# Optimization experiments

Measured on AMD Instinct MI355X. Metric: run time of the kernel, lower is better.

The kernel has to match this reference:

```python
import jax, jax.numpy as jnp
import numpy as np

N = 100000
E = 400000
G = 2000  # number of graphs in batch
IN_DIM = 32
H = 192
L = 4
EPS = 1e-5


def setup_inputs() -> dict:
    key = jax.random.key(0)
    ks = jax.random.split(key, 20)
    x = jax.random.normal(ks[0], (N, IN_DIM), jnp.float32)
    edge_src = jax.random.randint(ks[1], (E,), 0, N, jnp.int32)
    edge_dst = jax.random.randint(ks[2], (E,), 0, N, jnp.int32)
    batch = jnp.sort(jax.random.randint(ks[3], (N,), 0, G, jnp.int32))
    s_in = 1.0 / np.sqrt(IN_DIM)
    s_h = 1.0 / np.sqrt(H)
    return {
        "x": x,
        "edge_src": edge_src,
        "edge_dst": edge_dst,
        "batch": batch,
        # layer 0 (in_dim -> H); weights stored [in, out]
        "Wrel0": jax.random.uniform(ks[4], (IN_DIM, H), jnp.float32, -s_in, s_in),
        "brel0": jax.random.uniform(ks[5], (H,), jnp.float32, -s_in, s_in),
        "Wroot0": jax.random.uniform(ks[6], (IN_DIM, H), jnp.float32, -s_in, s_in),
        # layers 1..3 stacked (H -> H)
        "Wrel": jax.random.uniform(ks[7], (L - 1, H, H), jnp.float32, -s_h, s_h),
        "brel": jax.random.uniform(ks[8], (L - 1, H), jnp.float32, -s_h, s_h),
        "Wroot": jax.random.uniform(ks[9], (L - 1, H, H), jnp.float32, -s_h, s_h),
        # batchnorm affine params for all 4 layers
        "gamma": jnp.ones((L, H), jnp.float32),
        "beta": jnp.zeros((L, H), jnp.float32),
        # head MLP and output
        "Wh1": jax.random.uniform(ks[10], (H, H), jnp.float32, -s_h, s_h),
        "bh1": jax.random.uniform(ks[11], (H,), jnp.float32, -s_h, s_h),
        "Wh2": jax.random.uniform(ks[12], (H, H), jnp.float32, -s_h, s_h),
        "bh2": jax.random.uniform(ks[13], (H,), jnp.float32, -s_h, s_h),
        "Wout": jax.random.uniform(ks[14], (H, 1), jnp.float32, -s_h, s_h),
        "bout": jax.random.uniform(ks[15], (1,), jnp.float32, -s_h, s_h),
    }


def _rel_conv(x, edge_src, edge_dst, Wrel, brel, Wroot):
    # message: lin_rel(x_j); applying the linear at node level first is the
    # same math as per-edge (linear commutes with gather) and cheaper.
    h = x @ Wrel + brel                      # [N, out]
    agg = jax.ops.segment_sum(h[edge_src], edge_dst, num_segments=N)
    return agg + x @ Wroot


def _bn_relu(h, g, b):
    # BatchNorm1d in training mode: batch stats over node dim, biased var
    mu = h.mean(axis=0)
    var = jnp.var(h, axis=0)
    h = (h - mu) * jax.lax.rsqrt(var + EPS) * g + b
    return jax.nn.relu(h)


def reference(x, edge_src, edge_dst, batch, Wrel0, brel0, Wroot0,
              Wrel, brel, Wroot, gamma, beta, Wh1, bh1, Wh2, bh2, Wout, bout):
    h = _bn_relu(_rel_conv(x, edge_src, edge_dst, Wrel0, brel0, Wroot0),
                 gamma[0], beta[0])
    for i in range(L - 1):
        h = _bn_relu(_rel_conv(h, edge_src, edge_dst, Wrel[i], brel[i], Wroot[i]),
                     gamma[i + 1], beta[i + 1])
    # global mean pool over graphs
    sums = jax.ops.segment_sum(h, batch, num_segments=G)          # [G, H]
    cnt = jax.ops.segment_sum(jnp.ones((N,), h.dtype), batch, num_segments=G)
    g = sums / jnp.maximum(cnt, 1.0)[:, None]
    # head MLP (dropout is identity at eval) + output linear
    g = jax.nn.relu(g @ Wh1 + bh1) @ Wh2 + bh2
    return g @ Wout + bout                                        # [G, 1]
```

## Files before the change

kernel.cpp:

```cpp
#include <hip/hip_runtime.h>

#define HDIM 192
#define EPS 1e-5f

typedef __attribute__((ext_vector_type(8))) _Float16 half8;
typedef __attribute__((ext_vector_type(4))) float floatx4;

__device__ __forceinline__ float h2f(ushort u) {
    union { ushort u; _Float16 h; } c; c.u = u; return (float)c.h;
}
__device__ __forceinline__ ushort f2h(float x) {
    _Float16 h = (_Float16)x;
    union { _Float16 h; ushort u; } c; c.h = h; return c.u;
}
__device__ __forceinline__ uint4 pack8(const ushort* h) {
    uint4 p;
    p.x = h[0] | ((uint)h[1] << 16); p.y = h[2] | ((uint)h[3] << 16);
    p.z = h[4] | ((uint)h[5] << 16); p.w = h[6] | ((uint)h[7] << 16);
    return p;
}

__device__ __forceinline__ void gload_lds16(const ushort* g, ushort* l) {
    __builtin_amdgcn_global_load_lds(
        (const __attribute__((address_space(1))) unsigned int*)g,
        (__attribute__((address_space(3))) unsigned int*)l, 16, 0, 0);
}

#define WAITV0() asm volatile("s_waitcnt vmcnt(0)" ::: "memory")


struct PrepArgs {
    const float* src[6];
    ushort*      dst[6];
    int K[6];
    int off[7];
};

__global__ __launch_bounds__(256) void prep_all_k(PrepArgs a)
{
    int idx = blockIdx.x * 256 + threadIdx.x;
    if (idx >= a.off[6]) return;
    int i = 0;
    #pragma unroll
    for (int t = 1; t < 6; ++t) if (idx >= a.off[t]) i = t;
    int r = idx - a.off[i];
    int K = a.K[i];
    int perMat = (K >> 5) * 12 * 64;
    int mat = r / perMat;
    r -= mat * perMat;
    int lane = r & 63;
    int ct = (r >> 6) % 12;
    int kc = r / (12 * 64);
    int col = ct * 16 + (lane & 15);
    int kb  = kc * 32 + (lane >> 4) * 8;
    const float* Wm = a.src[i] + (size_t)mat * K * HDIM;
    ushort* base = a.dst[i] + (size_t)mat * K * HDIM;
    size_t o = (size_t)kc * 6144 + (size_t)(ct * 64 + lane) * 8;
    #pragma unroll
    for (int j = 0; j < 8; ++j)
        base[o + j] = f2h(Wm[(size_t)(kb + j) * HDIM + col]);
}

__global__ __launch_bounds__(256) void conv_half_k(
    const float* __restrict__ src, ushort* __restrict__ dst, int R, int C)
{
    int OC = C >> 3;
    int idx = blockIdx.x * 256 + threadIdx.x;
    if (idx >= R * OC) return;
    int r = idx / OC;
    int o = idx - r * OC;
    float4 v0 = ((const float4*)(src + (size_t)r * C + o * 8))[0];
    float4 v1 = ((const float4*)(src + (size_t)r * C + o * 8))[1];
    float v[8] = {v0.x, v0.y, v0.z, v0.w, v1.x, v1.y, v1.z, v1.w};
    ushort h[8];
    #pragma unroll
    for (int t = 0; t < 8; ++t) h[t] = f2h(v[t]);
    *(uint4*)(dst + (size_t)r * C + o * 8) = pack8(h);
}

template<bool DUAL, bool RELU, bool DEG, bool STATS, bool BNIN, int NKC>
__global__ __launch_bounds__(256, 3) void gemm_mfma_k(
    const ushort* __restrict__ A1h, const ushort* __restrict__ W1f,
    const ushort* __restrict__ A2h, const ushort* __restrict__ W2f,
    const float* __restrict__ degf, const float* __restrict__ bias,
    const float* __restrict__ instats, const float* __restrict__ gammaL,
    const float* __restrict__ betaL, float invN,
    ushort* __restrict__ C, float* __restrict__ pstats, int N, int K)
{
    constexpr int KR   = NKC * 32;
    constexpr int RS   = KR + 8;
    constexpr int SLAB = 64 * RS;
    constexpr int NINSTR = SLAB / 512;
    constexpr int NCH  = DUAL ? 2 * NKC : NKC;
    constexpr int SMEMU = ((DUAL ? 2 * SLAB : SLAB) > 12800)
                            ? (DUAL ? 2 * SLAB : SLAB) : 12800;

    __shared__ float sstat[2][HDIM];
    __shared__ __align__(16) ushort smem[SMEMU];
    const int tid  = threadIdx.x;
    const int wave = tid >> 6;
    const int lane = tid & 63;
    const int row0 = blockIdx.x * 64;
    const int m16 = lane & 15;
    const int g4  = lane >> 4;

    if (STATS && !BNIN && tid < HDIM) { sstat[0][tid] = 0.f; sstat[1][tid] = 0.f; }

    auto stage = [&](const ushort* Ab, int slabOff) {
        #pragma unroll
        for (int i = wave; i < NINSTR; i += 4) {
            int slotB = i * 1024 + lane * 16;
            int r   = slotB / (RS * 2);
            int off = slotB - r * (RS * 2);
            if (off >= KR * 2) off = KR * 2 - 16;
            int rr = row0 + r; if (rr >= N) rr = N - 1;
            gload_lds16(Ab + (size_t)rr * KR + (off >> 1),
                        smem + slabOff + i * 512);
        }
    };

    stage(A1h, 0);
    if constexpr (DUAL) stage(A2h, SLAB);
    WAITV0();
    __builtin_amdgcn_s_barrier();
    __builtin_amdgcn_sched_barrier(0);

    if constexpr (BNIN) {
        if (tid < HDIM) {
            float mu  = instats[tid] * invN;
            float var = instats[HDIM + tid] * invN - mu * mu;
            float s = gammaL[tid] * rsqrtf(var + EPS);
            sstat[0][tid] = s;
            sstat[1][tid] = betaL[tid] - mu * s;
        }
        __syncthreads();
        {
            int r = tid >> 2, q = tid & 3;
            ushort* rowp = smem + SLAB + r * RS + q * 48;
            #pragma unroll
            for (int k = 0; k < 6; ++k) {
                uint4 hv = *(uint4*)(rowp + k * 8);
                uint hu[4] = {hv.x, hv.y, hv.z, hv.w};
                ushort oh[8];
                #pragma unroll
                for (int e = 0; e < 4; ++e) {
                    int ch = q * 48 + k * 8 + e * 2;
                    float v0 = h2f((ushort)(hu[e] & 0xffffu)) * sstat[0][ch]     + sstat[1][ch];
                    float v1 = h2f((ushort)(hu[e] >> 16))     * sstat[0][ch + 1] + sstat[1][ch + 1];
                    oh[2*e]   = f2h(fmaxf(v0, 0.f));
                    oh[2*e+1] = f2h(fmaxf(v1, 0.f));
                }
                *(uint4*)(rowp + k * 8) = pack8(oh);
            }
        }
        __syncthreads();
        if (STATS && tid < HDIM) { sstat[0][tid] = 0.f; sstat[1][tid] = 0.f; }
    }

    auto loadB = [&](int c, half8* b) {
        bool ph = DUAL && (c >= NKC);
        int kc = ph ? c - NKC : c;
        const ushort* Bp = (ph ? W2f : W1f) + (size_t)kc * 6144
                         + (size_t)(wave * 192 + lane) * 8;
        #pragma unroll
        for (int ct = 0; ct < 3; ++ct)
            b[ct] = *(const half8*)(Bp + ct * 512);
    };

    floatx4 acc[4][3];
    #pragma unroll
    for (int s = 0; s < 4; ++s)
        #pragma unroll
        for (int ct = 0; ct < 3; ++ct) acc[s][ct] = (floatx4){0.f, 0.f, 0.f, 0.f};

    half8 bA[3], bB[3];
    loadB(0, bA);
    #pragma unroll
    for (int c = 0; c < NCH; ++c) {
        if (c + 1 < NCH) loadB(c + 1, (c & 1) ? bA : bB);
        const int base = (DUAL && c >= NKC) ? SLAB : 0;
        const int kc   = (DUAL && c >= NKC) ? c - NKC : c;
        const ushort* aB = smem + base + m16 * RS + kc * 32 + g4 * 8;
        half8 a[4];
        #pragma unroll
        for (int s = 0; s < 4; ++s)
            a[s] = *(const half8*)(aB + s * 16 * RS);
        const half8* bu = (c & 1) ? bB : bA;
        #pragma unroll
        for (int ct = 0; ct < 3; ++ct)
            #pragma unroll
            for (int s = 0; s < 4; ++s)
                acc[s][ct] = __builtin_amdgcn_mfma_f32_16x16x32_f16(a[s], bu[ct], acc[s][ct], 0, 0, 0);
    }

    __syncthreads();
    #pragma unroll
    for (int ct = 0; ct < 3; ++ct) {
        int col = wave * 48 + ct * 16 + m16;
        float bv = bias ? bias[col] : 0.f;
        float lsum = 0.f, lsq = 0.f;
        #pragma unroll
        for (int s = 0; s < 4; ++s) {
            #pragma unroll
            for (int reg = 0; reg < 4; ++reg) {
                int rloc = s * 16 + g4 * 4 + reg;
                int rr = row0 + rloc;
                int rrc = rr < N ? rr : N - 1;
                float v = acc[s][ct][reg] + (DEG ? degf[rrc] * bv : bv);
                if (STATS && rr < N) { lsum += v; lsq += v * v; }
                if (RELU) v = fmaxf(v, 0.f);
                smem[rloc * 200 + col] = f2h(v);
            }
        }
        if (STATS) {
            lsum += __shfl_xor(lsum, 16); lsum += __shfl_xor(lsum, 32);
            lsq  += __shfl_xor(lsq, 16);  lsq  += __shfl_xor(lsq, 32);
            if (g4 == 0) {
                atomicAdd(&sstat[0][col], lsum);
                atomicAdd(&sstat[1][col], lsq);
            }
        }
    }
    __syncthreads();
    {
        int rowsLeft = N - row0; if (rowsLeft > 64) rowsLeft = 64;
        int lim = rowsLeft * 24;
        ushort* Cb = C + (size_t)row0 * HDIM;
        #pragma unroll
        for (int k = 0; k < 6; ++k) {
            int u = tid + k * 256;
            if (u < lim) {
                int r  = u / 24;
                int c8 = (u - r * 24) * 8;
                *(uint4*)(Cb + (size_t)u * 8) =
                    *(const uint4*)(smem + r * 200 + c8);
            }
        }
    }
    if (STATS) {
        if (tid < HDIM) {
            float* pb = pstats + (size_t)blockIdx.x * (2 * HDIM);
            pb[tid]        = sstat[0][tid];
            pb[HDIM + tid] = sstat[1][tid];
        }
    }
}

__global__ __launch_bounds__(256) void bn_reduce_k(
    const float* __restrict__ pbuf, float* __restrict__ stats, int nb)
{
    __shared__ float red[32][9];
    int t  = threadIdx.x;
    int cl = t & 7;
    int s  = t >> 3;
    int c  = blockIdx.x * 8 + cl;
    float acc = 0.f;
    int b = s;
    for (; b + 96 < nb; b += 128) {
        float a0 = pbuf[(size_t)b * 384 + c];
        float a1 = pbuf[(size_t)(b + 32) * 384 + c];
        float a2 = pbuf[(size_t)(b + 64) * 384 + c];
        float a3 = pbuf[(size_t)(b + 96) * 384 + c];
        acc += a0 + a1 + a2 + a3;
    }
    for (; b < nb; b += 32)
        acc += pbuf[(size_t)b * 384 + c];
    red[s][cl] = acc;
    __syncthreads();
    if (t < 8) {
        float a = 0.f;
        #pragma unroll
        for (int i = 0; i < 32; ++i) a += red[i][t];
        stats[blockIdx.x * 8 + t] = a;
    }
}

__global__ __launch_bounds__(256) void hist_k(
    const int* __restrict__ dst, int* __restrict__ deg, int E)
{
    int e = blockIdx.x * 256 + threadIdx.x;
    if (e < E) atomicAdd(&deg[dst[e]], 1);
}

__global__ __launch_bounds__(256) void block_sum_k(
    const int* __restrict__ deg, int* __restrict__ bsum, int N)
{
    __shared__ int s[256];
    int t = threadIdx.x;
    int n = blockIdx.x * 256 + t;
    s[t] = (n < N) ? deg[n] : 0;
    __syncthreads();
    for (int off = 128; off > 0; off >>= 1) {
        if (t < off) s[t] += s[t + off];
        __syncthreads();
    }
    if (t == 0) bsum[blockIdx.x] = s[0];
}

__global__ __launch_bounds__(512) void scan_bsum_k(int* __restrict__ bsum, int nb)
{
    __shared__ int s[512];
    int t = threadIdx.x;
    int v = (t < nb) ? bsum[t] : 0;
    s[t] = v;
    __syncthreads();
    for (int off = 1; off < 512; off <<= 1) {
        int u = (t >= off) ? s[t - off] : 0;
        __syncthreads();
        s[t] += u;
        __syncthreads();
    }
    if (t < nb) bsum[t] = s[t] - v;
}

__global__ __launch_bounds__(256) void row_ptr_k(
    const int* __restrict__ deg, const int* __restrict__ bsum,
    int* __restrict__ row_ptr, int* __restrict__ cursor,
    float* __restrict__ degf, int N, int E)
{
    __shared__ int s[256];
    int t = threadIdx.x;
    int n = blockIdx.x * 256 + t;
    int v = (n < N) ? deg[n] : 0;
    s[t] = v;
    __syncthreads();
    for (int off = 1; off < 256; off <<= 1) {
        int u = (t >= off) ? s[t - off] : 0;
        __syncthreads();
        s[t] += u;
        __syncthreads();
    }
    int ex = s[t] - v + bsum[blockIdx.x];
    if (n < N) {
        row_ptr[n] = ex;
        cursor[n]  = ex;
        degf[n]    = (float)v;
    }
    if (blockIdx.x == 0 && t == 0) row_ptr[N] = E;
}

__global__ __launch_bounds__(256) void fill_k(
    const int* __restrict__ src, const int* __restrict__ dst,
    int* __restrict__ cursor, int* __restrict__ col, int E)
{
    int e = blockIdx.x * 256 + threadIdx.x;
    if (e < E) {
        int p = atomicAdd(&cursor[dst[e]], 1);
        col[p] = src[e];
    }
}

__global__ __launch_bounds__(256) void gather_h_k(
    const ushort* __restrict__ xh, const int* __restrict__ row_ptr,
    const int* __restrict__ col, ushort* __restrict__ gh, int N, int K)
{
    int OC = K >> 3;
    int idx = blockIdx.x * 256 + threadIdx.x;
    if (idx >= N * OC) return;
    int n = idx / OC;
    int o = idx - n * OC;
    const ushort* hp = xh + o * 8;
    int j0 = row_ptr[n], j1 = row_ptr[n + 1];
    float acc[8] = {0.f,0.f,0.f,0.f,0.f,0.f,0.f,0.f};
    auto addrow = [&](uint4 hv) {
        uint hu[4] = {hv.x, hv.y, hv.z, hv.w};
        #pragma unroll
        for (int t = 0; t < 4; ++t) {
            acc[2*t]   += h2f((ushort)(hu[t] & 0xffffu));
            acc[2*t+1] += h2f((ushort)(hu[t] >> 16));
        }
    };
    int j = j0;
    for (; j + 3 < j1; j += 4) {
        int s0 = col[j], s1 = col[j+1], s2 = col[j+2], s3 = col[j+3];
        uint4 v0 = *(const uint4*)(hp + (size_t)s0 * K);
        uint4 v1 = *(const uint4*)(hp + (size_t)s1 * K);
        uint4 v2 = *(const uint4*)(hp + (size_t)s2 * K);
        uint4 v3 = *(const uint4*)(hp + (size_t)s3 * K);
        addrow(v0); addrow(v1); addrow(v2); addrow(v3);
    }
    for (; j < j1; ++j)
        addrow(*(const uint4*)(hp + (size_t)col[j] * K));
    ushort oh[8];
    #pragma unroll
    for (int t = 0; t < 8; ++t) oh[t] = f2h(acc[t]);
    *(uint4*)(gh + (size_t)n * K + o * 8) = pack8(oh);
}

__global__ __launch_bounds__(256) void gather_bn_k(
    const ushort* __restrict__ h, const float* __restrict__ stats,
    const float* __restrict__ gamma, const float* __restrict__ beta,
    float invN, const int* __restrict__ row_ptr, const int* __restrict__ col,
    ushort* __restrict__ gh, int N)
{
    int idx = blockIdx.x * 256 + threadIdx.x;
    if (idx >= N * 24) return;
    int n = idx / 24;
    int o = idx - n * 24;
    int q = o * 8;
    float sc[8], sh[8];
    #pragma unroll
    for (int t = 0; t < 8; ++t) {
        float mu  = stats[q + t] * invN;
        float var = stats[HDIM + q + t] * invN - mu * mu;
        float s = gamma[q + t] * rsqrtf(var + EPS);
        sc[t] = s; sh[t] = beta[q + t] - mu * s;
    }
    const ushort* hp = h + q;
    int j0 = row_ptr[n], j1 = row_ptr[n + 1];
    float acc[8] = {0.f,0.f,0.f,0.f,0.f,0.f,0.f,0.f};
    auto addrow = [&](uint4 hv) {
        uint hu[4] = {hv.x, hv.y, hv.z, hv.w};
        #pragma unroll
        for (int t = 0; t < 4; ++t) {
            float v0 = h2f((ushort)(hu[t] & 0xffffu));
            float v1 = h2f((ushort)(hu[t] >> 16));
            acc[2*t]   += fmaxf(v0 * sc[2*t]   + sh[2*t],   0.f);
            acc[2*t+1] += fmaxf(v1 * sc[2*t+1] + sh[2*t+1], 0.f);
        }
    };
    int j = j0;
    for (; j + 3 < j1; j += 4) {
        int s0 = col[j], s1 = col[j+1], s2 = col[j+2], s3 = col[j+3];
        uint4 v0 = *(const uint4*)(hp + (size_t)s0 * HDIM);
        uint4 v1 = *(const uint4*)(hp + (size_t)s1 * HDIM);
        uint4 v2 = *(const uint4*)(hp + (size_t)s2 * HDIM);
        uint4 v3 = *(const uint4*)(hp + (size_t)s3 * HDIM);
        addrow(v0); addrow(v1); addrow(v2); addrow(v3);
    }
    for (; j < j1; ++j)
        addrow(*(const uint4*)(hp + (size_t)col[j] * HDIM));
    ushort oh[8];
    #pragma unroll
    for (int t = 0; t < 8; ++t) oh[t] = f2h(acc[t]);
    *(uint4*)(gh + (size_t)n * HDIM + q) = pack8(oh);
}

__global__ __launch_bounds__(192) void pool_bn_k(
    const ushort* __restrict__ h, const float* __restrict__ stats,
    const float* __restrict__ gamma, const float* __restrict__ beta,
    float invN, const int* __restrict__ batch,
    ushort* __restrict__ gsh, int G, int N)
{
    __shared__ int bounds[2];
    int g = blockIdx.x;
    int c = threadIdx.x;
    if (c < 2) {
        int key = g + c;
        int lo = 0, hi = N;
        while (lo < hi) {
            int mid = (lo + hi) >> 1;
            if (batch[mid] < key) lo = mid + 1; else hi = mid;
        }
        bounds[c] = lo;
    }
    __syncthreads();
    int r0 = bounds[0], r1 = bounds[1];
    float mu  = stats[c] * invN;
    float var = stats[HDIM + c] * invN - mu * mu;
    float sc  = gamma[c] * rsqrtf(var + EPS);
    float sh  = beta[c] - mu * sc;
    const ushort* base = h + c;
    float s = 0.f;
    for (int r = r0; r < r1; ++r)
        s += fmaxf(h2f(base[(size_t)r * HDIM]) * sc + sh, 0.f);
    float m = s / fmaxf((float)(r1 - r0), 1.f);
    gsh[(size_t)g * HDIM + c] = f2h(m);
}

__global__ __launch_bounds__(64) void out_dot_k(
    const ushort* __restrict__ g2h, const float* __restrict__ Wout,
    const float* __restrict__ bout, float* __restrict__ out, int G)
{
    int gi = blockIdx.x;
    int t = threadIdx.x;
    float s = 0.f;
    #pragma unroll
    for (int j = 0; j < 3; ++j) {
        int c = t + j * 64;
        s += h2f(g2h[(size_t)gi * HDIM + c]) * Wout[c];
    }
    #pragma unroll
    for (int off = 32; off > 0; off >>= 1) s += __shfl_down(s, off, 64);
    if (t == 0) out[gi] = s + bout[0];
}

extern "C" void kernel_launch(void* const* d_in, const int* in_sizes, int n_in,
                              void* d_out, int out_size, void* d_ws, size_t ws_size,
                              hipStream_t stream)
{
    const float* x      = (const float*)d_in[0];
    const int*   esrc   = (const int*)d_in[1];
    const int*   edst   = (const int*)d_in[2];
    const int*   batch  = (const int*)d_in[3];
    const float* Wrel0  = (const float*)d_in[4];
    const float* brel0  = (const float*)d_in[5];
    const float* Wroot0 = (const float*)d_in[6];
    const float* Wrel   = (const float*)d_in[7];
    const float* brel   = (const float*)d_in[8];
    const float* Wroot  = (const float*)d_in[9];
    const float* gamma  = (const float*)d_in[10];
    const float* beta   = (const float*)d_in[11];
    const float* Wh1    = (const float*)d_in[12];
    const float* bh1    = (const float*)d_in[13];
    const float* Wh2    = (const float*)d_in[14];
    const float* bh2    = (const float*)d_in[15];
    const float* Wout   = (const float*)d_in[16];
    const float* bout   = (const float*)d_in[17];
    float* out = (float*)d_out;

    const int N  = in_sizes[3];
    const int E  = in_sizes[1];
    const int K0 = in_sizes[0] / N;
    const int G  = out_size;
    const int nBlocks = (N + 255) / 256;
    const float invN = 1.0f / (float)N;

    char* p = (char*)d_ws;
    auto carve = [&](size_t bytes) -> void* {
        void* r = (void*)p; p += (bytes + 255) & ~(size_t)255; return r;
    };
    ushort* bufa_h= (ushort*)carve((size_t)N * HDIM * 2);
    ushort* xh    = (ushort*)carve((size_t)N * HDIM * 2);
    ushort* gh    = (ushort*)carve((size_t)N * HDIM * 2);
    ushort* gsh   = (ushort*)carve((size_t)G * HDIM * 2);
    ushort* g1h   = (ushort*)carve((size_t)G * HDIM * 2);
    ushort* g2h   = (ushort*)carve((size_t)G * HDIM * 2);
    int*    deg   = (int*)   carve((size_t)N * 4);
    float*  bnsums= (float*) carve(4 * 2 * HDIM * 4);
    size_t  zspan = (char*)(bnsums + 4 * 2 * HDIM) - (char*)deg;
    float*  degf  = (float*) carve((size_t)N * 4);
    int*    row_ptr=(int*)   carve((size_t)(N + 1) * 4);
    int*    cursor= (int*)   carve((size_t)N * 4);
    int*    col   = (int*)   carve((size_t)E * 4);
    int*    bsum  = (int*)   carve((size_t)nBlocks * 4);
    ushort* Wrel0f= (ushort*)carve((size_t)K0 * HDIM * 2);
    ushort* Wroot0f=(ushort*)carve((size_t)K0 * HDIM * 2);
    ushort* Wrelf = (ushort*)carve((size_t)3 * HDIM * HDIM * 2);
    ushort* Wrootf= (ushort*)carve((size_t)3 * HDIM * HDIM * 2);
    ushort* Wh1f  = (ushort*)carve((size_t)HDIM * HDIM * 2);
    ushort* Wh2f  = (ushort*)carve((size_t)HDIM * HDIM * 2);

    dim3 b256(256);
    const int eBlocks = (E + 255) / 256;
    const int gemmN = (N + 63) / 64;
    const int gemmG = (G + 63) / 64;

    float*  pbuf  = (float*) carve((size_t)gemmN * 2 * HDIM * 4);

    {
        PrepArgs a;
        int t0 = (K0 >> 5) * 12 * 64;
        int t1 = (HDIM >> 5) * 12 * 64;
        a.src[0] = Wrel0;  a.dst[0] = Wrel0f;  a.K[0] = K0;
        a.src[1] = Wroot0; a.dst[1] = Wroot0f; a.K[1] = K0;
        a.src[2] = Wrel;   a.dst[2] = Wrelf;   a.K[2] = HDIM;
        a.src[3] = Wroot;  a.dst[3] = Wrootf;  a.K[3] = HDIM;
        a.src[4] = Wh1;    a.dst[4] = Wh1f;    a.K[4] = HDIM;
        a.src[5] = Wh2;    a.dst[5] = Wh2f;    a.K[5] = HDIM;
        a.off[0] = 0;
        a.off[1] = a.off[0] + t0;
        a.off[2] = a.off[1] + t0;
        a.off[3] = a.off[2] + 3 * t1;
        a.off[4] = a.off[3] + 3 * t1;
        a.off[5] = a.off[4] + t1;
        a.off[6] = a.off[5] + t1;
        prep_all_k<<<(a.off[6] + 255) / 256, b256, 0, stream>>>(a);
    }
    conv_half_k<<<((N * (K0 >> 3)) + 255) / 256, b256, 0, stream>>>(x, xh, N, K0);

    hipMemsetAsync(deg, 0, zspan, stream);
    hist_k<<<eBlocks, b256, 0, stream>>>(edst, deg, E);
    block_sum_k<<<nBlocks, b256, 0, stream>>>(deg, bsum, N);
    scan_bsum_k<<<1, dim3(512), 0, stream>>>(bsum, nBlocks);
    row_ptr_k<<<nBlocks, b256, 0, stream>>>(deg, bsum, row_ptr, cursor, degf, N, E);
    fill_k<<<eBlocks, b256, 0, stream>>>(esrc, edst, cursor, col, E);

    gather_h_k<<<((N * (K0 >> 3)) + 255) / 256, b256, 0, stream>>>(
        xh, row_ptr, col, gh, N, K0);
    gemm_mfma_k<true, false, true, true, false, 1><<<gemmN, b256, 0, stream>>>(
        gh, Wrel0f, xh, Wroot0f, degf, brel0,
        nullptr, nullptr, nullptr, 0.f, bufa_h, pbuf, N, K0);
    bn_reduce_k<<<48, b256, 0, stream>>>(pbuf, bnsums, gemmN);

    for (int l = 1; l < 4; ++l) {
        const ushort* Wrf = Wrelf  + (size_t)(l - 1) * HDIM * HDIM;
        const ushort* Wtf = Wrootf + (size_t)(l - 1) * HDIM * HDIM;
        const float*  br  = brel   + (size_t)(l - 1) * HDIM;
        const float*  st  = bnsums + (size_t)(l - 1) * 2 * HDIM;
        const float*  gm  = gamma  + (size_t)(l - 1) * HDIM;
        const float*  bt  = beta   + (size_t)(l - 1) * HDIM;
        gather_bn_k<<<(N * 24 + 255) / 256, b256, 0, stream>>>(
            bufa_h, st, gm, bt, invN, row_ptr, col, gh, N);
        gemm_mfma_k<true, false, true, true, true, 6><<<gemmN, b256, 0, stream>>>(
            gh, Wrf, bufa_h, Wtf, degf, br,
            st, gm, bt, invN, bufa_h, pbuf, N, HDIM);
        bn_reduce_k<<<48, b256, 0, stream>>>(pbuf, bnsums + l * 2 * HDIM, gemmN);
    }

    pool_bn_k<<<G, dim3(192), 0, stream>>>(
        bufa_h, bnsums + 3 * 2 * HDIM, gamma + 3 * HDIM, beta + 3 * HDIM,
        invN, batch, gsh, G, N);

    gemm_mfma_k<false, true, false, false, false, 6><<<gemmG, b256, 0, stream>>>(
        gsh, Wh1f, nullptr, nullptr, nullptr, bh1,
        nullptr, nullptr, nullptr, 0.f, g1h, nullptr, G, HDIM);
    gemm_mfma_k<false, false, false, false, false, 6><<<gemmG, b256, 0, stream>>>(
        g1h, Wh2f, nullptr, nullptr, nullptr, bh2,
        nullptr, nullptr, nullptr, 0.f, g2h, nullptr, G, HDIM);
    out_dot_k<<<G, dim3(64), 0, stream>>>(g2h, Wout, bout, out, G);
}
```

Before: 456.1 us.

## Fuse BN-ReLU neighbor gather into hidden-layer dual GEMM kernel

```diff
diff --git a/kernel.cpp b/kernel.cpp
--- a/kernel.cpp
+++ b/kernel.cpp
@@ -78,13 +78,11 @@
     *(uint4*)(dst + (size_t)r * C + o * 8) = pack8(h);
 }
 
-template<bool DUAL, bool RELU, bool DEG, bool STATS, bool BNIN, int NKC>
+template<bool DUAL, bool RELU, bool DEG, bool STATS, int NKC>
 __global__ __launch_bounds__(256, 3) void gemm_mfma_k(
     const ushort* __restrict__ A1h, const ushort* __restrict__ W1f,
     const ushort* __restrict__ A2h, const ushort* __restrict__ W2f,
     const float* __restrict__ degf, const float* __restrict__ bias,
-    const float* __restrict__ instats, const float* __restrict__ gammaL,
-    const float* __restrict__ betaL, float invN,
     ushort* __restrict__ C, float* __restrict__ pstats, int N, int K)
 {
     constexpr int KR   = NKC * 32;
@@ -104,7 +102,7 @@
     const int m16 = lane & 15;
     const int g4  = lane >> 4;
 
-    if (STATS && !BNIN && tid < HDIM) { sstat[0][tid] = 0.f; sstat[1][tid] = 0.f; }
+    if (STATS && tid < HDIM) { sstat[0][tid] = 0.f; sstat[1][tid] = 0.f; }
 
     auto stage = [&](const ushort* Ab, int slabOff) {
         #pragma unroll
@@ -124,38 +122,6 @@
     WAITV0();
     __builtin_amdgcn_s_barrier();
     __builtin_amdgcn_sched_barrier(0);
-
-    if constexpr (BNIN) {
-        if (tid < HDIM) {
-            float mu  = instats[tid] * invN;
-            float var = instats[HDIM + tid] * invN - mu * mu;
-            float s = gammaL[tid] * rsqrtf(var + EPS);
-            sstat[0][tid] = s;
-            sstat[1][tid] = betaL[tid] - mu * s;
-        }
-        __syncthreads();
-        {
-            int r = tid >> 2, q = tid & 3;
-            ushort* rowp = smem + SLAB + r * RS + q * 48;
-            #pragma unroll
-            for (int k = 0; k < 6; ++k) {
-                uint4 hv = *(uint4*)(rowp + k * 8);
-                uint hu[4] = {hv.x, hv.y, hv.z, hv.w};
-                ushort oh[8];
-                #pragma unroll
-                for (int e = 0; e < 4; ++e) {
-                    int ch = q * 48 + k * 8 + e * 2;
-                    float v0 = h2f((ushort)(hu[e] & 0xffffu)) * sstat[0][ch]     + sstat[1][ch];
-                    float v1 = h2f((ushort)(hu[e] >> 16))     * sstat[0][ch + 1] + sstat[1][ch + 1];
-                    oh[2*e]   = f2h(fmaxf(v0, 0.f));
-                    oh[2*e+1] = f2h(fmaxf(v1, 0.f));
-                }
-                *(uint4*)(rowp + k * 8) = pack8(oh);
-            }
-        }
-        __syncthreads();
-        if (STATS && tid < HDIM) { sstat[0][tid] = 0.f; sstat[1][tid] = 0.f; }
-    }
 
     auto loadB = [&](int c, half8* b) {
         bool ph = DUAL && (c >= NKC);
@@ -243,6 +209,194 @@
             pb[tid]        = sstat[0][tid];
             pb[HDIM + tid] = sstat[1][tid];
         }
+    }
+}
+
+__global__ __launch_bounds__(256, 3) void gemm_fused_k(
+    const ushort* __restrict__ Hraw, const ushort* __restrict__ W1f,
+    const ushort* __restrict__ W2f,
+    const float* __restrict__ degf, const float* __restrict__ bias,
+    const float* __restrict__ instats, const float* __restrict__ gammaL,
+    const float* __restrict__ betaL, float invN,
+    const int* __restrict__ row_ptr, const int* __restrict__ col,
+    ushort* __restrict__ C, float* __restrict__ pstats, int N)
+{
+    constexpr int KR   = 192;
+    constexpr int RS   = 200;
+    constexpr int SLAB = 64 * RS;
+    constexpr int NINSTR = SLAB / 512;
+    constexpr int NKC  = 6, NCH = 12;
+
+    __shared__ float sstat[2][HDIM];
+    __shared__ __align__(16) ushort smem[2 * SLAB];
+    const int tid  = threadIdx.x;
+    const int wave = tid >> 6;
+    const int lane = tid & 63;
+    const int row0 = blockIdx.x * 64;
+    const int m16 = lane & 15;
+    const int g4  = lane >> 4;
+
+    #pragma unroll
+    for (int i = wave; i < NINSTR; i += 4) {
+        int slotB = i * 1024 + lane * 16;
+        int r   = slotB / (RS * 2);
+        int off = slotB - r * (RS * 2);
+        if (off >= KR * 2) off = KR * 2 - 16;
+        int rr = row0 + r; if (rr >= N) rr = N - 1;
+        gload_lds16(Hraw + (size_t)rr * KR + (off >> 1),
+                    smem + SLAB + i * 512);
+    }
+    WAITV0();
+    __builtin_amdgcn_s_barrier();
+    __builtin_amdgcn_sched_barrier(0);
+
+    if (tid < HDIM) {
+        float mu  = instats[tid] * invN;
+        float var = instats[HDIM + tid] * invN - mu * mu;
+        float s = gammaL[tid] * rsqrtf(var + EPS);
+        sstat[0][tid] = s;
+        sstat[1][tid] = betaL[tid] - mu * s;
+    }
+    __syncthreads();
+
+    const int r = tid >> 2, q = tid & 3;
+    {
+        ushort* rowp = smem + SLAB + r * RS + q * 48;
+        #pragma unroll
+        for (int k = 0; k < 6; ++k) {
+            uint4 hv = *(uint4*)(rowp + k * 8);
+            uint hu[4] = {hv.x, hv.y, hv.z, hv.w};
+            ushort oh[8];
+            #pragma unroll
+            for (int e = 0; e < 4; ++e) {
+                int ch = q * 48 + k * 8 + e * 2;
+                float v0 = h2f((ushort)(hu[e] & 0xffffu)) * sstat[0][ch]     + sstat[1][ch];
+                float v1 = h2f((ushort)(hu[e] >> 16))     * sstat[0][ch + 1] + sstat[1][ch + 1];
+                oh[2*e]   = f2h(fmaxf(v0, 0.f));
+                oh[2*e+1] = f2h(fmaxf(v1, 0.f));
+            }
+            *(uint4*)(rowp + k * 8) = pack8(oh);
+        }
+    }
+    {
+        float acc[48];
+        #pragma unroll
+        for (int i = 0; i < 48; ++i) acc[i] = 0.f;
+        int rr = row0 + r;
+        if (rr < N) {
+            int j0 = row_ptr[rr], j1 = row_ptr[rr + 1];
+            const ushort* hp = Hraw + q * 48;
+            for (int j = j0; j < j1; ++j) {
+                int s = col[j];
+                const ushort* rp = hp + (size_t)s * KR;
+                #pragma unroll
+                for (int ck = 0; ck < 6; ++ck) {
+                    uint4 hv = *(const uint4*)(rp + ck * 8);
+                    uint hu[4] = {hv.x, hv.y, hv.z, hv.w};
+                    #pragma unroll
+                    for (int e = 0; e < 4; ++e) {
+                        int ch = q * 48 + ck * 8 + e * 2;
+                        float v0 = h2f((ushort)(hu[e] & 0xffffu)) * sstat[0][ch]     + sstat[1][ch];
+                        float v1 = h2f((ushort)(hu[e] >> 16))     * sstat[0][ch + 1] + sstat[1][ch + 1];
+                        acc[ck*8 + e*2]     += fmaxf(v0, 0.f);
+                        acc[ck*8 + e*2 + 1] += fmaxf(v1, 0.f);
+                    }
+                }
+            }
+        }
+        ushort* dst = smem + r * RS + q * 48;
+        #pragma unroll
+        for (int ck = 0; ck < 6; ++ck) {
+            ushort oh[8];
+            #pragma unroll
+            for (int e = 0; e < 8; ++e) oh[e] = f2h(acc[ck*8 + e]);
+            *(uint4*)(dst + ck * 8) = pack8(oh);
+        }
+    }
+    __syncthreads();
+    if (tid < HDIM) { sstat[0][tid] = 0.f; sstat[1][tid] = 0.f; }
+
+    auto loadB = [&](int c, half8* b) {
+        bool ph = (c >= NKC);
+        int kc = ph ? c - NKC : c;
+        const ushort* Bp = (ph ? W2f : W1f) + (size_t)kc * 6144
+                         + (size_t)(wave * 192 + lane) * 8;
+        #pragma unroll
+        for (int ct = 0; ct < 3; ++ct)
+            b[ct] = *(const half8*)(Bp + ct * 512);
+    };
+
+    floatx4 acc[4][3];
+    #pragma unroll
+    for (int s = 0; s < 4; ++s)
+        #pragma unroll
+        for (int ct = 0; ct < 3; ++ct) acc[s][ct] = (floatx4){0.f, 0.f, 0.f, 0.f};
+
+    half8 bA[3], bB[3];
+    loadB(0, bA);
+    #pragma unroll
+    for (int c = 0; c < NCH; ++c) {
+        if (c + 1 < NCH) loadB(c + 1, (c & 1) ? bA : bB);
+        const int base = (c >= NKC) ? SLAB : 0;
+        const int kc   = (c >= NKC) ? c - NKC : c;
+        const ushort* aB = smem + base + m16 * RS + kc * 32 + g4 * 8;
+        half8 a[4];
+        #pragma unroll
+        for (int s = 0; s < 4; ++s)
+            a[s] = *(const half8*)(aB + s * 16 * RS);
+        const half8* bu = (c & 1) ? bB : bA;
+        #pragma unroll
+        for (int ct = 0; ct < 3; ++ct)
+            #pragma unroll
+            for (int s = 0; s < 4; ++s)
+                acc[s][ct] = __builtin_amdgcn_mfma_f32_16x16x32_f16(a[s], bu[ct], acc[s][ct], 0, 0, 0);
+    }
+
+    __syncthreads();
+    #pragma unroll
+    for (int ct = 0; ct < 3; ++ct) {
+        int colc = wave * 48 + ct * 16 + m16;
+        float bv = bias[colc];
+        float lsum = 0.f, lsq = 0.f;
+        #pragma unroll
+        for (int s = 0; s < 4; ++s) {
+            #pragma unroll
+            for (int reg = 0; reg < 4; ++reg) {
+                int rloc = s * 16 + g4 * 4 + reg;
+                int rr = row0 + rloc;
+                int rrc = rr < N ? rr : N - 1;
+                float v = acc[s][ct][reg] + degf[rrc] * bv;
+                if (rr < N) { lsum += v; lsq += v * v; }
+                smem[rloc * 200 + colc] = f2h(v);
+            }
+        }
+        lsum += __shfl_xor(lsum, 16); lsum += __shfl_xor(lsum, 32);
+        lsq  += __shfl_xor(lsq, 16);  lsq  += __shfl_xor(lsq, 32);
+        if (g4 == 0) {
+            atomicAdd(&sstat[0][colc], lsum);
+            atomicAdd(&sstat[1][colc], lsq);
+        }
+    }
+    __syncthreads();
+    {
+        int rowsLeft = N - row0; if (rowsLeft > 64) rowsLeft = 64;
+        int lim = rowsLeft * 24;
+        ushort* Cb = C + (size_t)row0 * HDIM;
+        #pragma unroll
+        for (int k = 0; k < 6; ++k) {
+            int u = tid + k * 256;
+            if (u < lim) {
+                int rr = u / 24;
+                int c8 = (u - rr * 24) * 8;
+                *(uint4*)(Cb + (size_t)u * 8) =
+                    *(const uint4*)(smem + rr * 200 + c8);
+            }
+        }
+    }
+    if (tid < HDIM) {
+        float* pb = pstats + (size_t)blockIdx.x * (2 * HDIM);
+        pb[tid]        = sstat[0][tid];
+        pb[HDIM + tid] = sstat[1][tid];
     }
 }
 
@@ -385,55 +539,6 @@
     #pragma unroll
     for (int t = 0; t < 8; ++t) oh[t] = f2h(acc[t]);
     *(uint4*)(gh + (size_t)n * K + o * 8) = pack8(oh);
-}
-
-__global__ __launch_bounds__(256) void gather_bn_k(
-    const ushort* __restrict__ h, const float* __restrict__ stats,
-    const float* __restrict__ gamma, const float* __restrict__ beta,
-    float invN, const int* __restrict__ row_ptr, const int* __restrict__ col,
-    ushort* __restrict__ gh, int N)
-{
-    int idx = blockIdx.x * 256 + threadIdx.x;
-    if (idx >= N * 24) return;
-    int n = idx / 24;
-    int o = idx - n * 24;
-    int q = o * 8;
-    float sc[8], sh[8];
-    #pragma unroll
-    for (int t = 0; t < 8; ++t) {
-        float mu  = stats[q + t] * invN;
-        float var = stats[HDIM + q + t] * invN - mu * mu;
-        float s = gamma[q + t] * rsqrtf(var + EPS);
-        sc[t] = s; sh[t] = beta[q + t] - mu * s;
-    }
-    const ushort* hp = h + q;
-    int j0 = row_ptr[n], j1 = row_ptr[n + 1];
-    float acc[8] = {0.f,0.f,0.f,0.f,0.f,0.f,0.f,0.f};
-    auto addrow = [&](uint4 hv) {
-        uint hu[4] = {hv.x, hv.y, hv.z, hv.w};
-        #pragma unroll
-        for (int t = 0; t < 4; ++t) {
-            float v0 = h2f((ushort)(hu[t] & 0xffffu));
-            float v1 = h2f((ushort)(hu[t] >> 16));
-            acc[2*t]   += fmaxf(v0 * sc[2*t]   + sh[2*t],   0.f);
-            acc[2*t+1] += fmaxf(v1 * sc[2*t+1] + sh[2*t+1], 0.f);
-        }
-    };
-    int j = j0;
-    for (; j + 3 < j1; j += 4) {
-        int s0 = col[j], s1 = col[j+1], s2 = col[j+2], s3 = col[j+3];
-        uint4 v0 = *(const uint4*)(hp + (size_t)s0 * HDIM);
-        uint4 v1 = *(const uint4*)(hp + (size_t)s1 * HDIM);
-        uint4 v2 = *(const uint4*)(hp + (size_t)s2 * HDIM);
-        uint4 v3 = *(const uint4*)(hp + (size_t)s3 * HDIM);
-        addrow(v0); addrow(v1); addrow(v2); addrow(v3);
-    }
-    for (; j < j1; ++j)
-        addrow(*(const uint4*)(hp + (size_t)col[j] * HDIM));
-    ushort oh[8];
-    #pragma unroll
-    for (int t = 0; t < 8; ++t) oh[t] = f2h(acc[t]);
-    *(uint4*)(gh + (size_t)n * HDIM + q) = pack8(oh);
 }
 
 __global__ __launch_bounds__(192) void pool_bn_k(
@@ -521,8 +626,9 @@
         void* r = (void*)p; p += (bytes + 255) & ~(size_t)255; return r;
     };
     ushort* bufa_h= (ushort*)carve((size_t)N * HDIM * 2);
-    ushort* xh    = (ushort*)carve((size_t)N * HDIM * 2);
-    ushort* gh    = (ushort*)carve((size_t)N * HDIM * 2);
+    ushort* bufb_h= (ushort*)carve((size_t)N * HDIM * 2);
+    ushort* xh    = (ushort*)carve((size_t)N * K0 * 2);
+    ushort* gh    = (ushort*)carve((size_t)N * K0 * 2);
     ushort* gsh   = (ushort*)carve((size_t)G * HDIM * 2);
     ushort* g1h   = (ushort*)carve((size_t)G * HDIM * 2);
     ushort* g2h   = (ushort*)carve((size_t)G * HDIM * 2);
@@ -578,11 +684,12 @@
 
     gather_h_k<<<((N * (K0 >> 3)) + 255) / 256, b256, 0, stream>>>(
         xh, row_ptr, col, gh, N, K0);
-    gemm_mfma_k<true, false, true, true, false, 1><<<gemmN, b256, 0, stream>>>(
-        gh, Wrel0f, xh, Wroot0f, degf, brel0,
-        nullptr, nullptr, nullptr, 0.f, bufa_h, pbuf, N, K0);
+    gemm_mfma_k<true, false, true, true, 1><<<gemmN, b256, 0, stream>>>(
+        gh, Wrel0f, xh, Wroot0f, degf, brel0, bufa_h, pbuf, N, K0);
     bn_reduce_k<<<48, b256, 0, stream>>>(pbuf, bnsums, gemmN);
 
+    ushort* rd = bufa_h;
+    ushort* wr = bufb_h;
     for (int l = 1; l < 4; ++l) {
         const ushort* Wrf = Wrelf  + (size_t)(l - 1) * HDIM * HDIM;
         const ushort* Wtf = Wrootf + (size_t)(l - 1) * HDIM * HDIM;
@@ -590,23 +697,20 @@
         const float*  st  = bnsums + (size_t)(l - 1) * 2 * HDIM;
         const float*  gm  = gamma  + (size_t)(l - 1) * HDIM;
         const float*  bt  = beta   + (size_t)(l - 1) * HDIM;
-        gather_bn_k<<<(N * 24 + 255) / 256, b256, 0, stream>>>(
-            bufa_h, st, gm, bt, invN, row_ptr, col, gh, N);
-        gemm_mfma_k<true, false, true, true, true, 6><<<gemmN, b256, 0, stream>>>(
-            gh, Wrf, bufa_h, Wtf, degf, br,
-            st, gm, bt, invN, bufa_h, pbuf, N, HDIM);
+        gemm_fused_k<<<gemmN, b256, 0, stream>>>(
+            rd, Wrf, Wtf, degf, br, st, gm, bt, invN,
+            row_ptr, col, wr, pbuf, N);
         bn_reduce_k<<<48, b256, 0, stream>>>(pbuf, bnsums + l * 2 * HDIM, gemmN);
+        ushort* tmp = rd; rd = wr; wr = tmp;
     }
 
     pool_bn_k<<<G, dim3(192), 0, stream>>>(
-        bufa_h, bnsums + 3 * 2 * HDIM, gamma + 3 * HDIM, beta + 3 * HDIM,
+        rd, bnsums + 3 * 2 * HDIM, gamma + 3 * HDIM, beta + 3 * HDIM,
         invN, batch, gsh, G, N);
 
-    gemm_mfma_k<false, true, false, false, false, 6><<<gemmG, b256, 0, stream>>>(
-        gsh, Wh1f, nullptr, nullptr, nullptr, bh1,
-        nullptr, nullptr, nullptr, 0.f, g1h, nullptr, G, HDIM);
-    gemm_mfma_k<false, false, false, false, false, 6><<<gemmG, b256, 0, stream>>>(
-        g1h, Wh2f, nullptr, nullptr, nullptr, bh2,
-        nullptr, nullptr, nullptr, 0.f, g2h, nullptr, G, HDIM);
+    gemm_mfma_k<false, true, false, false, 6><<<gemmG, b256, 0, stream>>>(
+        gsh, Wh1f, nullptr, nullptr, nullptr, bh1, g1h, nullptr, G, HDIM);
+    gemm_mfma_k<false, false, false, false, 6><<<gemmG, b256, 0, stream>>>(
+        g1h, Wh2f, nullptr, nullptr, nullptr, bh2, g2h, nullptr, G, HDIM);
     out_dot_k<<<G, dim3(64), 0, stream>>>(g2h, Wout, bout, out, G);
 }
```

Measured after the change: 474.3 us. +4.0%, slower.
